# Performance work log

Hardware: AMD Instinct MI355X
Metric: run time of the kernel (lower is better)

The kernel has to match this reference:

```python
import jax, jax.numpy as jnp
import numpy as np

H = 256      # hidden_dim
F_IN = 32    # infeat_dim1 + infeat_dim2 (shared 'feat')
P = 8192     # nodes per topo level
L = 16       # topo levels; level 0 = PIs, last level = POs
FANIN = 8    # uniform in-degree (dense mailbox)


def _mlp(x, w1, b1, w2, b2):
    # MLP(sizes...) = Linear -> LeakyReLU(0.1) -> Linear
    return jax.nn.leaky_relu(x @ w1 + b1, 0.1) @ w2 + b2


def setup_inputs() -> dict:
    key = jax.random.key(0)
    ks = jax.random.split(key, 24)
    w = lambda k, s: jax.random.normal(k, s, jnp.float32) * 0.1
    z = lambda n: jnp.zeros((n,), jnp.float32)
    return {
        "delay": jax.random.uniform(ks[0], (P, 1), jnp.float32),
        "feat": jax.random.normal(ks[1], (L * P, F_IN), jnp.float32),
        "bit_pos": jax.random.uniform(ks[2], (L - 1, P, FANIN), jnp.float32),
        "po_feat": jax.random.uniform(ks[3], (P, 1), jnp.float32),
        "src_idx": jax.random.randint(ks[4], (L - 1, P, FANIN), 0, P, jnp.int32),
        # mlp_pi: 1 -> H/2 -> H
        "pi_w1": w(ks[5], (1, H // 2)), "pi_b1": z(H // 2),
        "pi_w2": w(ks[6], (H // 2, H)), "pi_b2": z(H),
        # mlp_neigh_gate: (H + F_IN) -> H/2 -> H
        "gate_w1": w(ks[7], (H + F_IN, H // 2)), "gate_b1": z(H // 2),
        "gate_w2": w(ks[8], (H // 2, H)), "gate_b2": z(H),
        # mlp_neigh_module: (H + F_IN + 1) -> H/2 -> H
        "mod_w1": w(ks[9], (H + F_IN + 1, H // 2)), "mod_b1": z(H // 2),
        "mod_w2": w(ks[10], (H // 2, H)), "mod_b2": z(H),
        # mlp_type: F_IN -> 32 -> 32
        "type_w1": w(ks[11], (F_IN, 32)), "type_b1": z(32),
        "type_w2": w(ks[12], (32, 32)), "type_b2": z(32),
        # mlp_pos: 1 -> 32 -> 32
        "pos_w1": w(ks[13], (1, 32)), "pos_b1": z(32),
        "pos_w2": w(ks[14], (32, 32)), "pos_b2": z(32),
        "attn_vec_m": w(ks[15], (H + 64, 1)),
        # mlp_global: 1 -> H/2 -> H
        "glob_w1": w(ks[16], (1, H // 2)), "glob_b1": z(H // 2),
        "glob_w2": w(ks[17], (H // 2, H)), "glob_b2": z(H),
        # mlp_out: 2H -> H -> 1
        "out_w1": w(ks[18], (2 * H, H)), "out_b1": z(H),
        "out_w2": w(ks[19], (H, 1)), "out_b2": z(1),
    }


def reference(delay, feat, bit_pos, po_feat,
              pi_w1, pi_b1, pi_w2, pi_b2,
              gate_w1, gate_b1, gate_w2, gate_b2,
              mod_w1, mod_b1, mod_w2, mod_b2,
              type_w1, type_b1, type_w2, type_b2,
              pos_w1, pos_b1, pos_w2, pos_b2,
              attn_vec_m,
              glob_w1, glob_b1, glob_w2, glob_b2,
              out_w1, out_b1, out_w2, out_b2,
              src_idx):
    L1, P_, F_ = src_idx.shape  # levels beyond PIs
    Pg = P_ // 2                # first half gates, second half modules
    # level 0: nodes_func_pi -> h = mlp_pi(delay)
    prev_h = _mlp(delay, pi_w1, pi_b1, pi_w2, pi_b2)  # [P, H]
    for l in range(L1):
        sh = prev_h[src_idx[l]]                    # gather src h: [P, F, H]
        lvl_feat = feat[(l + 1) * P_:(l + 2) * P_]  # [P, F_IN]
        # --- gates: reduce_func_smoothmax + nodes_func_gate ---
        mg = sh[:Pg]                               # mailbox [Pg, F, H]
        neigh_g = jnp.sum(mg * jax.nn.softmax(mg, axis=1), axis=1)  # [Pg, H]
        hg = _mlp(jnp.concatenate([neigh_g, lvl_feat[:Pg]], axis=1),
                  gate_w1, gate_b1, gate_w2, gate_b2)
        # --- modules: edge_msg_module + reduce_func_attn + nodes_func_module ---
        sm = sh[Pg:]                               # [Pm, F, H]
        dstf = lvl_feat[Pg:]                       # [Pm, F_IN]
        zt = _mlp(dstf, type_w1, type_b1, type_w2, type_b2)          # [Pm, 32]
        bp = bit_pos[l, Pg:]                       # [Pm, F]
        zp = _mlp(bp[..., None], pos_w1, pos_b1, pos_w2, pos_b2)     # [Pm, F, 32]
        z = jnp.concatenate(
            [jnp.broadcast_to(zt[:, None, :], zp.shape), zp, sm], axis=-1)  # [Pm, F, H+64]
        alpha = jax.nn.softmax(z @ attn_vec_m, axis=1)               # [Pm, F, 1]
        m = jnp.concatenate([sm, bp[..., None]], axis=-1)            # [Pm, F, H+1]
        neigh_m = jnp.sum(alpha * m, axis=1)                         # [Pm, H+1]
        hm = _mlp(jnp.concatenate([neigh_m, dstf], axis=1),
                  mod_w1, mod_b1, mod_w2, mod_b2)
        hl = jnp.concatenate([hg, hm], axis=0)     # [P, H]
        # ReLU where is_po != 1; only last level nodes are POs
        prev_h = hl if l == L1 - 1 else jax.nn.relu(hl)
    # POs = entire last level; flag_global concat
    h_global = _mlp(po_feat, glob_w1, glob_b1, glob_w2, glob_b2)  # [P, H]
    h = jnp.concatenate([prev_h, h_global], axis=1)               # [P, 2H]
    return _mlp(h, out_w1, out_b1, out_w2, out_b2)                # [P, 1]
```

## Files before the change

kernel.cpp:

```cpp
#include <hip/hip_runtime.h>
#include <math.h>

#define HD   256
#define FIN  32
#define NP   8192
#define PGH  4096
#define NLVL 15
#define TN   16

typedef __attribute__((ext_vector_type(4))) short v4s;
typedef __attribute__((ext_vector_type(8))) short v8s;
typedef __attribute__((ext_vector_type(4))) float v4f;

#define MFMA __builtin_amdgcn_mfma_f32_16x16x32_bf16

__device__ __align__(16) unsigned short g_wpk[606208];

__device__ __forceinline__ float lrelu(float x) { return x > 0.f ? x : 0.1f * x; }

__device__ __forceinline__ void cvt_duo(float v, unsigned short& hi, unsigned short& lo) {
    unsigned int u = __float_as_uint(v);
    unsigned int r = u + 0x7fffu + ((u >> 16) & 1u);
    hi = (unsigned short)(r >> 16);
    float d = v - __uint_as_float((unsigned int)hi << 16);
    unsigned int u2 = __float_as_uint(d);
    unsigned int r2 = u2 + 0x7fffu + ((u2 >> 16) & 1u);
    lo = (unsigned short)(r2 >> 16);
}

__device__ __forceinline__ v8s pack8(v4s a, v4s b) {
    v8s r; r[0]=a[0]; r[1]=a[1]; r[2]=a[2]; r[3]=a[3]; r[4]=b[0]; r[5]=b[1]; r[6]=b[2]; r[7]=b[3];
    return r;
}

__global__ __launch_bounds__(256) void prep_kernel(
    const float* __restrict__ gw1, const float* __restrict__ mw1,
    const float* __restrict__ gw2, const float* __restrict__ mw2,
    const float* __restrict__ glw2, const float* __restrict__ ow1)
{
    int t = blockIdx.x * 256 + threadIdx.x;
    const float* src; int base, N, idx;
    if (t < 36864)       { src = gw1;  base = 0;      N = 128; idx = t; }
    else if (t < 73728)  { src = mw1;  base = 73728;  N = 128; idx = t - 36864; }
    else if (t < 106496) { src = gw2;  base = 147456; N = 256; idx = t - 73728; }
    else if (t < 139264) { src = mw2;  base = 212992; N = 256; idx = t - 106496; }
    else if (t < 172032) { src = glw2; base = 278528; N = 256; idx = t - 139264; }
    else if (t < 303104) { src = ow1;  base = 344064; N = 256; idx = t - 172032; }
    else return;
    int sh = (N == 128) ? 7 : 8;
    int k = idx >> sh, col = idx & (N - 1);
    float v = src[idx];
    unsigned short hi, lo; cvt_duo(v, hi, lo);
    int ks = k >> 5, kk = k & 31;
    int ch = col >> 7, cc = col & 127, ct = cc >> 4;
    int nch = N >> 7;
    int l = ((kk & 15) >> 2) * 16 + (cc & 15);
    int w = (kk & 3) + (kk >> 4) * 4;
    int off = ((ks * nch + ch) * 2) * 4096 + ct * 512 + l * 8 + w;
    g_wpk[base + off] = hi;
    g_wpk[base + off + 4096] = lo;
}

__global__ __launch_bounds__(256) void pi_kernel(
    const float* __restrict__ delay,
    const float* __restrict__ w1, const float* __restrict__ b1,
    const float* __restrict__ w2, const float* __restrict__ b2,
    const float* __restrict__ av,
    float* __restrict__ outh, float* __restrict__ sdot)
{
    __shared__ float g1[TN][132];
    const int tid = threadIdx.x;
    const int node0 = blockIdx.x * TN;

    for (int t = tid; t < TN * 128; t += 256) {
        int i = t >> 7, jj = t & 127;
        g1[i][jj] = lrelu(delay[node0 + i] * w1[jj] + b1[jj]);
    }
    __syncthreads();

    const int j = (tid & 63) * 4;
    const int rg = (tid >> 6) * 4;
    float acc[4][4];
    float4 bv = *(const float4*)&b2[j];
#pragma unroll
    for (int ri = 0; ri < 4; ri++) { acc[ri][0] = bv.x; acc[ri][1] = bv.y; acc[ri][2] = bv.z; acc[ri][3] = bv.w; }

#pragma unroll 2
    for (int k = 0; k < 128; k += 4) {
        float4 x0 = *(const float4*)&g1[rg + 0][k];
        float4 x1 = *(const float4*)&g1[rg + 1][k];
        float4 x2v = *(const float4*)&g1[rg + 2][k];
        float4 x3 = *(const float4*)&g1[rg + 3][k];
        const float* wp = w2 + (size_t)k * 256 + j;
#define PIK(comp, off) { float4 wv = *(const float4*)(wp + (off) * 256); \
    acc[0][0] += x0.comp * wv.x; acc[0][1] += x0.comp * wv.y; acc[0][2] += x0.comp * wv.z; acc[0][3] += x0.comp * wv.w; \
    acc[1][0] += x1.comp * wv.x; acc[1][1] += x1.comp * wv.y; acc[1][2] += x1.comp * wv.z; acc[1][3] += x1.comp * wv.w; \
    acc[2][0] += x2v.comp * wv.x; acc[2][1] += x2v.comp * wv.y; acc[2][2] += x2v.comp * wv.z; acc[2][3] += x2v.comp * wv.w; \
    acc[3][0] += x3.comp * wv.x; acc[3][1] += x3.comp * wv.y; acc[3][2] += x3.comp * wv.z; acc[3][3] += x3.comp * wv.w; }
        PIK(x, 0) PIK(y, 1) PIK(z, 2) PIK(w, 3)
#undef PIK
    }
    float4 avj = *(const float4*)&av[64 + j];
#pragma unroll
    for (int ri = 0; ri < 4; ri++) {
        *(float4*)&outh[(node0 + rg + ri) * HD + j] =
            make_float4(acc[ri][0], acc[ri][1], acc[ri][2], acc[ri][3]);
        float p = acc[ri][0] * avj.x + acc[ri][1] * avj.y + acc[ri][2] * avj.z + acc[ri][3] * avj.w;
#pragma unroll
        for (int off = 1; off < 64; off <<= 1) p += __shfl_xor(p, off);
        if ((tid & 63) == 0) sdot[node0 + rg + ri] = p;
    }
}

__global__ __launch_bounds__(512, 4) void level_kernel(
    const float* __restrict__ prevh, float* __restrict__ nexth,
    const float* __restrict__ sdot_prev, float* __restrict__ sdot_next,
    const float* __restrict__ feat, const float* __restrict__ bitpos,
    const int* __restrict__ srcidx,
    const float* __restrict__ g_w1, const float* __restrict__ g_b1,
    const float* __restrict__ g_b2,
    const float* __restrict__ m_w1, const float* __restrict__ m_b1,
    const float* __restrict__ m_b2,
    const float* __restrict__ t_w1, const float* __restrict__ t_b1,
    const float* __restrict__ t_w2, const float* __restrict__ t_b2,
    const float* __restrict__ p_w1, const float* __restrict__ p_b1,
    const float* __restrict__ p_w2, const float* __restrict__ p_b2,
    const float* __restrict__ av,
    int level, int apply_relu)
{
    __shared__ unsigned short xh_lds[16 * 296];
    __shared__ unsigned short xl_lds[16 * 296];
    __shared__ unsigned short h1h_lds[16 * 136];
    __shared__ unsigned short h1l_lds[16 * 136];
    __shared__ float wbuf[2][4096];
    __shared__ int   src_lds[128];
    __shared__ float bp_lds[128];
    __shared__ float dstf_lds[16][32];
    __shared__ float ztt_lds[16][32];
    __shared__ float alpha_lds[128];
    __shared__ float xbp_lds[16];
    __shared__ float av_lds[64];
    __shared__ float tw2av_lds[32];
    __shared__ float pw2av_lds[32];
    __shared__ float bias_av[2];
    __shared__ float red_lds[16][8];

    const int tid = threadIdx.x;
    const bool is_gate = (blockIdx.x < 256);
    const int node0 = is_gate ? (blockIdx.x * TN) : (PGH + ((int)blockIdx.x - 256) * TN);

    const float* w1 = is_gate ? g_w1 : m_w1;
    const float* b1 = is_gate ? g_b1 : m_b1;
    const float* b2 = is_gate ? g_b2 : m_b2;
    const float4* gpk1 = (const float4*)(g_wpk + (is_gate ? 0 : 73728));
    const float4* gpk2 = (const float4*)(g_wpk + (is_gate ? 147456 : 212992));

    float4 ta = gpk1[tid], tb = gpk1[512 + tid];

    if (tid < 128) src_lds[tid] = srcidx[(level * NP + node0) * 8 + tid];

    if (is_gate) {
        {
            int i = tid >> 5, k = tid & 31;
            float v = feat[((level + 1) * NP + node0 + i) * FIN + k];
            unsigned short h, l; cvt_duo(v, h, l);
            xh_lds[i * 296 + 256 + k] = h; xl_lds[i * 296 + 256 + k] = l;
        }
        __syncthreads();
        {
            const int c = tid & 255, sh = (tid >> 8) * 8;
            for (int s0 = 0; s0 < 8; s0 += 4) {
                const int* spA = &src_lds[(sh + s0 + 0) * 8];
                const int* spB = &src_lds[(sh + s0 + 1) * 8];
                const int* spC = &src_lds[(sh + s0 + 2) * 8];
                const int* spD = &src_lds[(sh + s0 + 3) * 8];
                float ma[8], mb[8], mc[8], md[8];
#pragma unroll
                for (int f = 0; f < 8; f++) ma[f] = prevh[spA[f] * HD + c];
#pragma unroll
                for (int f = 0; f < 8; f++) mb[f] = prevh[spB[f] * HD + c];
#pragma unroll
                for (int f = 0; f < 8; f++) mc[f] = prevh[spC[f] * HD + c];
#pragma unroll
                for (int f = 0; f < 8; f++) md[f] = prevh[spD[f] * HD + c];
                float mxa = -1e30f, mxb = -1e30f, mxc = -1e30f, mxd = -1e30f;
#pragma unroll
                for (int f = 0; f < 8; f++) {
                    mxa = fmaxf(mxa, ma[f]); mxb = fmaxf(mxb, mb[f]);
                    mxc = fmaxf(mxc, mc[f]); mxd = fmaxf(mxd, md[f]);
                }
                float sa = 0.f, wsa = 0.f, sb = 0.f, wsb = 0.f;
                float sc = 0.f, wsc = 0.f, sd = 0.f, wsd = 0.f;
#pragma unroll
                for (int f = 0; f < 8; f++) {
                    float ea = __expf(ma[f] - mxa); sa += ea; wsa += ma[f] * ea;
                    float eb = __expf(mb[f] - mxb); sb += eb; wsb += mb[f] * eb;
                    float ec = __expf(mc[f] - mxc); sc += ec; wsc += mc[f] * ec;
                    float ed = __expf(md[f] - mxd); sd += ed; wsd += md[f] * ed;
                }
                unsigned short h, l;
                cvt_duo(wsa / sa, h, l); xh_lds[(sh+s0+0)*296 + c] = h; xl_lds[(sh+s0+0)*296 + c] = l;
                cvt_duo(wsb / sb, h, l); xh_lds[(sh+s0+1)*296 + c] = h; xl_lds[(sh+s0+1)*296 + c] = l;
                cvt_duo(wsc / sc, h, l); xh_lds[(sh+s0+2)*296 + c] = h; xl_lds[(sh+s0+2)*296 + c] = l;
                cvt_duo(wsd / sd, h, l); xh_lds[(sh+s0+3)*296 + c] = h; xl_lds[(sh+s0+3)*296 + c] = l;
            }
        }
        __syncthreads();
    } else {
        if (tid < 128) bp_lds[tid] = bitpos[(level * NP + node0) * 8 + tid];
        {
            int i = tid >> 5, k = tid & 31;
            float v = feat[((level + 1) * NP + node0 + i) * FIN + k];
            dstf_lds[i][k] = v;
            unsigned short h, l; cvt_duo(v, h, l);
            xh_lds[i * 296 + 257 + k] = h; xl_lds[i * 296 + 257 + k] = l;
        }
        if (tid < 64) av_lds[tid] = av[tid];
        __syncthreads();

        {
            int i = tid >> 5, jj = tid & 31;
            float a = t_b1[jj];
#pragma unroll 8
            for (int k = 0; k < 32; k++) a += dstf_lds[i][k] * t_w1[k * 32 + jj];
            ztt_lds[i][jj] = lrelu(a);
        }
        if (tid < 32) {
            float s = 0.f;
#pragma unroll 8
            for (int jj = 0; jj < 32; jj++) s += t_w2[tid * 32 + jj] * av_lds[jj];
            tw2av_lds[tid] = s;
        } else if (tid < 64) {
            int k = tid - 32;
            float s = 0.f;
#pragma unroll 8
            for (int jj = 0; jj < 32; jj++) s += p_w2[k * 32 + jj] * av_lds[32 + jj];
            pw2av_lds[k] = s;
        } else if (tid == 64) {
            float s = 0.f;
#pragma unroll 8
            for (int jj = 0; jj < 32; jj++) s += t_b2[jj] * av_lds[jj];
            bias_av[0] = s;
        } else if (tid == 65) {
            float s = 0.f;
#pragma unroll 8
            for (int jj = 0; jj < 32; jj++) s += p_b2[jj] * av_lds[32 + jj];
            bias_av[1] = s;
        }
        __syncthreads();

        if (tid < 256) {
            const int jg = tid & 1, f = (tid >> 1) & 7, i = tid >> 4;
            const float sv = sdot_prev[src_lds[i * 8 + f]];
            const float bpv = bp_lds[i * 8 + f];
            float part = 0.f;
            const int k0 = jg * 16;
#pragma unroll
            for (int k = k0; k < k0 + 16; k++) {
                float h1pk = lrelu(bpv * p_w1[k] + p_b1[k]);
                part += h1pk * pw2av_lds[k];
                part += ztt_lds[i][k] * tw2av_lds[k];
            }
            part += __shfl_xor(part, 1);
            float logit = part + bias_av[0] + bias_av[1] + sv;
            float mx = logit;
            mx = fmaxf(mx, __shfl_xor(mx, 2));
            mx = fmaxf(mx, __shfl_xor(mx, 4));
            mx = fmaxf(mx, __shfl_xor(mx, 8));
            float e = __expf(logit - mx);
            float ssum = e;
            ssum += __shfl_xor(ssum, 2);
            ssum += __shfl_xor(ssum, 4);
            ssum += __shfl_xor(ssum, 8);
            float alpha = e / ssum;
            if (jg == 0) alpha_lds[i * 8 + f] = alpha;
            float ab = alpha * bpv;
            ab += __shfl_xor(ab, 2);
            ab += __shfl_xor(ab, 4);
            ab += __shfl_xor(ab, 8);
            if ((tid & 15) == 0) xbp_lds[i] = ab;
        }
        __syncthreads();

        {
            const int c = tid & 255, sh = (tid >> 8) * 8;
            for (int s0 = 0; s0 < 8; s0 += 4) {
                const int* spA = &src_lds[(sh + s0 + 0) * 8];
                const int* spB = &src_lds[(sh + s0 + 1) * 8];
                const int* spC = &src_lds[(sh + s0 + 2) * 8];
                const int* spD = &src_lds[(sh + s0 + 3) * 8];
                float ma[8], mb[8], mc[8], md[8];
#pragma unroll
                for (int f = 0; f < 8; f++) ma[f] = prevh[spA[f] * HD + c];
#pragma unroll
                for (int f = 0; f < 8; f++) mb[f] = prevh[spB[f] * HD + c];
#pragma unroll
                for (int f = 0; f < 8; f++) mc[f] = prevh[spC[f] * HD + c];
#pragma unroll
                for (int f = 0; f < 8; f++) md[f] = prevh[spD[f] * HD + c];
                const float* apA = &alpha_lds[(sh + s0 + 0) * 8];
                const float* apB = &alpha_lds[(sh + s0 + 1) * 8];
                const float* apC = &alpha_lds[(sh + s0 + 2) * 8];
                const float* apD = &alpha_lds[(sh + s0 + 3) * 8];
                float aa = 0.f, ab2 = 0.f, ac = 0.f, ad = 0.f;
#pragma unroll
                for (int f = 0; f < 8; f++) {
                    aa  += apA[f] * ma[f]; ab2 += apB[f] * mb[f];
                    ac  += apC[f] * mc[f]; ad  += apD[f] * md[f];
                }
                unsigned short h, l;
                cvt_duo(aa,  h, l); xh_lds[(sh+s0+0)*296 + c] = h; xl_lds[(sh+s0+0)*296 + c] = l;
                cvt_duo(ab2, h, l); xh_lds[(sh+s0+1)*296 + c] = h; xl_lds[(sh+s0+1)*296 + c] = l;
                cvt_duo(ac,  h, l); xh_lds[(sh+s0+2)*296 + c] = h; xl_lds[(sh+s0+2)*296 + c] = l;
                cvt_duo(ad,  h, l); xh_lds[(sh+s0+3)*296 + c] = h; xl_lds[(sh+s0+3)*296 + c] = l;
            }
        }
        if (tid < TN) {
            unsigned short h, l; cvt_duo(xbp_lds[tid], h, l);
            xh_lds[tid * 296 + 256] = h; xl_lds[tid * 296 + 256] = l;
        }
        __syncthreads();
    }

    const int lane = tid & 63, wv = tid >> 6;
    const int lr = lane & 15, lg = lane >> 4;

    {
        const unsigned short* xrh = xh_lds + lr * 296 + 4 * lg;
        const unsigned short* xrl = xl_lds + lr * 296 + 4 * lg;
        const int colg = wv * 16 + lr;
        float bb = b1[colg];
        v4f acc = {bb, bb, bb, bb};
        for (int s = 0; s < 9; ++s) {
            float4* w4 = (float4*)wbuf[s & 1];
            w4[tid] = ta; w4[tid + 512] = tb;
            if (s < 8) { ta = gpk1[(s + 1) * 1024 + tid]; tb = gpk1[(s + 1) * 1024 + 512 + tid]; }
            __syncthreads();
            const unsigned short* wb = (const unsigned short*)wbuf[s & 1];
            int k0 = s * 32;
            v8s Ah = pack8(*(const v4s*)(xrh + k0), *(const v4s*)(xrh + k0 + 16));
            v8s Al = pack8(*(const v4s*)(xrl + k0), *(const v4s*)(xrl + k0 + 16));
            v8s Bh = *(const v8s*)(wb + wv * 512 + lane * 8);
            v8s Bl = *(const v8s*)(wb + 4096 + wv * 512 + lane * 8);
            acc = MFMA(Ah, Bh, acc, 0, 0, 0);
            acc = MFMA(Ah, Bl, acc, 0, 0, 0);
            acc = MFMA(Al, Bh, acc, 0, 0, 0);
        }
        ta = gpk2[tid]; tb = gpk2[512 + tid];
        float w288 = is_gate ? 0.f : w1[288 * 128 + colg];
#pragma unroll
        for (int r = 0; r < 4; ++r) {
            int row = lg * 4 + r;
            float v = acc[r];
            if (!is_gate) v += dstf_lds[row][31] * w288;
            v = lrelu(v);
            unsigned short h, l; cvt_duo(v, h, l);
            h1h_lds[row * 136 + colg] = h;
            h1l_lds[row * 136 + colg] = l;
        }
    }
    __syncthreads();

    {
        const unsigned short* h1rh = h1h_lds + lr * 136 + 4 * lg;
        const unsigned short* h1rl = h1l_lds + lr * 136 + 4 * lg;
        const int col0 = wv * 16 + lr;
        float bb0 = b2[col0], bb1 = b2[128 + col0];
        v4f acc0 = {bb0, bb0, bb0, bb0};
        v4f acc1 = {bb1, bb1, bb1, bb1};
        v8s Ah = {0,0,0,0,0,0,0,0}, Al = {0,0,0,0,0,0,0,0};
#pragma unroll
        for (int s = 0; s < 8; ++s) {
            float4* w4 = (float4*)wbuf[s & 1];
            w4[tid] = ta; w4[tid + 512] = tb;
            if (s < 7) { ta = gpk2[(s + 1) * 1024 + tid]; tb = gpk2[(s + 1) * 1024 + 512 + tid]; }
            __syncthreads();
            const unsigned short* wb = (const unsigned short*)wbuf[s & 1];
            if ((s & 1) == 0) {
                int k0 = (s >> 1) * 32;
                Ah = pack8(*(const v4s*)(h1rh + k0), *(const v4s*)(h1rh + k0 + 16));
                Al = pack8(*(const v4s*)(h1rl + k0), *(const v4s*)(h1rl + k0 + 16));
            }
            v8s Bh = *(const v8s*)(wb + wv * 512 + lane * 8);
            v8s Bl = *(const v8s*)(wb + 4096 + wv * 512 + lane * 8);
            if ((s & 1) == 0) {
                acc0 = MFMA(Ah, Bh, acc0, 0, 0, 0);
                acc0 = MFMA(Ah, Bl, acc0, 0, 0, 0);
                acc0 = MFMA(Al, Bh, acc0, 0, 0, 0);
            } else {
                acc1 = MFMA(Ah, Bh, acc1, 0, 0, 0);
                acc1 = MFMA(Ah, Bl, acc1, 0, 0, 0);
                acc1 = MFMA(Al, Bh, acc1, 0, 0, 0);
            }
        }
        float pr[4] = {0.f, 0.f, 0.f, 0.f};
#pragma unroll
        for (int r = 0; r < 4; ++r) {
            int row = lg * 4 + r;
            float v = acc0[r];
            if (apply_relu) v = fmaxf(v, 0.f);
            nexth[(node0 + row) * HD + col0] = v;
            pr[r] += v * av[64 + col0];
            float v2 = acc1[r];
            if (apply_relu) v2 = fmaxf(v2, 0.f);
            nexth[(node0 + row) * HD + 128 + col0] = v2;
            pr[r] += v2 * av[192 + col0];
        }
#pragma unroll
        for (int off = 1; off < 16; off <<= 1) {
#pragma unroll
            for (int r = 0; r < 4; ++r) pr[r] += __shfl_xor(pr[r], off);
        }
        if (lr == 0) {
#pragma unroll
            for (int r = 0; r < 4; ++r) red_lds[lg * 4 + r][wv] = pr[r];
        }
        __syncthreads();
        if (tid < TN) {
            float s = 0.f;
#pragma unroll
            for (int w = 0; w < 8; w++) s += red_lds[tid][w];
            sdot_next[node0 + tid] = s;
        }
    }
}

__global__ __launch_bounds__(512, 4) void final_kernel(
    const float* __restrict__ prevh, const float* __restrict__ pofeat,
    const float* __restrict__ gl_w1, const float* __restrict__ gl_b1,
    const float* __restrict__ gl_b2,
    const float* __restrict__ o_b1,
    const float* __restrict__ o_w2, const float* __restrict__ o_b2,
    float* __restrict__ out)
{
    __shared__ unsigned short x2h[16 * 520];
    __shared__ unsigned short x2l[16 * 520];
    __shared__ unsigned short g1h[16 * 136];
    __shared__ unsigned short g1l[16 * 136];
    __shared__ float wbuf[2][4096];
    __shared__ float ow2_lds[256];
    __shared__ float red_lds[16][8];

    const int tid = threadIdx.x;
    const int node0 = blockIdx.x * TN;
    const float4* gpkG = (const float4*)(g_wpk + 278528);
    const float4* gpkO = (const float4*)(g_wpk + 344064);
    float4 ta = gpkG[tid], tb = gpkG[512 + tid];

    for (int q = tid; q < TN * 64; q += 512) {
        int i = q >> 6, c4 = (q & 63) * 4;
        float4 v = *(const float4*)&prevh[(node0 + i) * HD + c4];
        unsigned short h, l;
        cvt_duo(v.x, h, l); x2h[i * 520 + c4 + 0] = h; x2l[i * 520 + c4 + 0] = l;
        cvt_duo(v.y, h, l); x2h[i * 520 + c4 + 1] = h; x2l[i * 520 + c4 + 1] = l;
        cvt_duo(v.z, h, l); x2h[i * 520 + c4 + 2] = h; x2l[i * 520 + c4 + 2] = l;
        cvt_duo(v.w, h, l); x2h[i * 520 + c4 + 3] = h; x2l[i * 520 + c4 + 3] = l;
    }
    for (int t = tid; t < TN * 128; t += 512) {
        int i = t >> 7, jj = t & 127;
        float v = lrelu(pofeat[node0 + i] * gl_w1[jj] + gl_b1[jj]);
        unsigned short h, l; cvt_duo(v, h, l);
        g1h[i * 136 + jj] = h; g1l[i * 136 + jj] = l;
    }
    if (tid < 256) ow2_lds[tid] = o_w2[tid];
    __syncthreads();

    const int lane = tid & 63, wv = tid >> 6;
    const int lr = lane & 15, lg = lane >> 4;
    const int col0 = wv * 16 + lr;

    {
        const unsigned short* grh = g1h + lr * 136 + 4 * lg;
        const unsigned short* grl = g1l + lr * 136 + 4 * lg;
        float bb0 = gl_b2[col0], bb1 = gl_b2[128 + col0];
        v4f acc0 = {bb0, bb0, bb0, bb0};
        v4f acc1 = {bb1, bb1, bb1, bb1};
        v8s Ah = {0,0,0,0,0,0,0,0}, Al = {0,0,0,0,0,0,0,0};
#pragma unroll
        for (int s = 0; s < 8; ++s) {
            float4* w4 = (float4*)wbuf[s & 1];
            w4[tid] = ta; w4[tid + 512] = tb;
            if (s < 7) { ta = gpkG[(s + 1) * 1024 + tid]; tb = gpkG[(s + 1) * 1024 + 512 + tid]; }
            else       { ta = gpkO[tid]; tb = gpkO[512 + tid]; }
            __syncthreads();
            const unsigned short* wb = (const unsigned short*)wbuf[s & 1];
            if ((s & 1) == 0) {
                int k0 = (s >> 1) * 32;
                Ah = pack8(*(const v4s*)(grh + k0), *(const v4s*)(grh + k0 + 16));
                Al = pack8(*(const v4s*)(grl + k0), *(const v4s*)(grl + k0 + 16));
            }
            v8s Bh = *(const v8s*)(wb + wv * 512 + lane * 8);
            v8s Bl = *(const v8s*)(wb + 4096 + wv * 512 + lane * 8);
            if ((s & 1) == 0) {
                acc0 = MFMA(Ah, Bh, acc0, 0, 0, 0);
                acc0 = MFMA(Ah, Bl, acc0, 0, 0, 0);
                acc0 = MFMA(Al, Bh, acc0, 0, 0, 0);
            } else {
                acc1 = MFMA(Ah, Bh, acc1, 0, 0, 0);
                acc1 = MFMA(Ah, Bl, acc1, 0, 0, 0);
                acc1 = MFMA(Al, Bh, acc1, 0, 0, 0);
            }
        }
#pragma unroll
        for (int r = 0; r < 4; ++r) {
            int row = lg * 4 + r;
            unsigned short h, l;
            cvt_duo(acc0[r], h, l); x2h[row * 520 + 256 + col0] = h; x2l[row * 520 + 256 + col0] = l;
            cvt_duo(acc1[r], h, l); x2h[row * 520 + 384 + col0] = h; x2l[row * 520 + 384 + col0] = l;
        }
    }
    __syncthreads();

    {
        const unsigned short* xrh = x2h + lr * 520 + 4 * lg;
        const unsigned short* xrl = x2l + lr * 520 + 4 * lg;
        float bb0 = o_b1[col0], bb1 = o_b1[128 + col0];
        v4f acc0 = {bb0, bb0, bb0, bb0};
        v4f acc1 = {bb1, bb1, bb1, bb1};
        v8s Ah = {0,0,0,0,0,0,0,0}, Al = {0,0,0,0,0,0,0,0};
        for (int s = 0; s < 32; ++s) {
            float4* w4 = (float4*)wbuf[s & 1];
            w4[tid] = ta; w4[tid + 512] = tb;
            if (s < 31) { ta = gpkO[(s + 1) * 1024 + tid]; tb = gpkO[(s + 1) * 1024 + 512 + tid]; }
            __syncthreads();
            const unsigned short* wb = (const unsigned short*)wbuf[s & 1];
            if ((s & 1) == 0) {
                int k0 = (s >> 1) * 32;
                Ah = pack8(*(const v4s*)(xrh + k0), *(const v4s*)(xrh + k0 + 16));
                Al = pack8(*(const v4s*)(xrl + k0), *(const v4s*)(xrl + k0 + 16));
            }
            v8s Bh = *(const v8s*)(wb + wv * 512 + lane * 8);
            v8s Bl = *(const v8s*)(wb + 4096 + wv * 512 + lane * 8);
            if ((s & 1) == 0) {
                acc0 = MFMA(Ah, Bh, acc0, 0, 0, 0);
                acc0 = MFMA(Ah, Bl, acc0, 0, 0, 0);
                acc0 = MFMA(Al, Bh, acc0, 0, 0, 0);
            } else {
                acc1 = MFMA(Ah, Bh, acc1, 0, 0, 0);
                acc1 = MFMA(Ah, Bl, acc1, 0, 0, 0);
                acc1 = MFMA(Al, Bh, acc1, 0, 0, 0);
            }
        }
        float pr[4] = {0.f, 0.f, 0.f, 0.f};
#pragma unroll
        for (int r = 0; r < 4; ++r) {
            pr[r] += lrelu(acc0[r]) * ow2_lds[col0];
            pr[r] += lrelu(acc1[r]) * ow2_lds[128 + col0];
        }
#pragma unroll
        for (int off = 1; off < 16; off <<= 1) {
#pragma unroll
            for (int r = 0; r < 4; ++r) pr[r] += __shfl_xor(pr[r], off);
        }
        if (lr == 0) {
#pragma unroll
            for (int r = 0; r < 4; ++r) red_lds[lg * 4 + r][wv] = pr[r];
        }
        __syncthreads();
        if (tid < TN) {
            float s = 0.f;
#pragma unroll
            for (int w = 0; w < 8; w++) s += red_lds[tid][w];
            out[node0 + tid] = s + o_b2[0];
        }
    }
}

extern "C" void kernel_launch(void* const* d_in, const int* in_sizes, int n_in,
                              void* d_out, int out_size, void* d_ws, size_t ws_size,
                              hipStream_t stream)
{
    const float* delay    = (const float*)d_in[0];
    const float* feat     = (const float*)d_in[1];
    const float* bitpos   = (const float*)d_in[2];
    const float* pofeat   = (const float*)d_in[3];
    const int*   srcidx   = (const int*)  d_in[4];
    const float* pi_w1    = (const float*)d_in[5];
    const float* pi_b1    = (const float*)d_in[6];
    const float* pi_w2    = (const float*)d_in[7];
    const float* pi_b2    = (const float*)d_in[8];
    const float* gate_w1  = (const float*)d_in[9];
    const float* gate_b1  = (const float*)d_in[10];
    const float* gate_w2  = (const float*)d_in[11];
    const float* gate_b2  = (const float*)d_in[12];
    const float* mod_w1   = (const float*)d_in[13];
    const float* mod_b1   = (const float*)d_in[14];
    const float* mod_w2   = (const float*)d_in[15];
    const float* mod_b2   = (const float*)d_in[16];
    const float* type_w1  = (const float*)d_in[17];
    const float* type_b1  = (const float*)d_in[18];
    const float* type_w2  = (const float*)d_in[19];
    const float* type_b2  = (const float*)d_in[20];
    const float* pos_w1   = (const float*)d_in[21];
    const float* pos_b1   = (const float*)d_in[22];
    const float* pos_w2   = (const float*)d_in[23];
    const float* pos_b2   = (const float*)d_in[24];
    const float* attn_vec = (const float*)d_in[25];
    const float* glob_w1  = (const float*)d_in[26];
    const float* glob_b1  = (const float*)d_in[27];
    const float* glob_w2  = (const float*)d_in[28];
    const float* glob_b2  = (const float*)d_in[29];
    const float* out_w1   = (const float*)d_in[30];
    const float* out_b1   = (const float*)d_in[31];
    const float* out_w2   = (const float*)d_in[32];
    const float* out_b2   = (const float*)d_in[33];

    float* buf0 = (float*)d_ws;
    float* buf1 = buf0 + (size_t)NP * HD;
    float* sd0  = buf1 + (size_t)NP * HD;
    float* sd1  = sd0 + NP;

    prep_kernel<<<1184, 256, 0, stream>>>(gate_w1, mod_w1, gate_w2, mod_w2, glob_w2, out_w1);

    pi_kernel<<<NP / TN, 256, 0, stream>>>(delay, pi_w1, pi_b1, pi_w2, pi_b2,
                                           attn_vec, buf0, sd0);

    for (int l = 0; l < NLVL; l++) {
        float* pv = (l & 1) ? buf1 : buf0;
        float* nx = (l & 1) ? buf0 : buf1;
        float* sp = (l & 1) ? sd1 : sd0;
        float* sn = (l & 1) ? sd0 : sd1;
        level_kernel<<<NP / TN, 512, 0, stream>>>(
            pv, nx, sp, sn, feat, bitpos, srcidx,
            gate_w1, gate_b1, gate_b2,
            mod_w1, mod_b1, mod_b2,
            type_w1, type_b1, type_w2, type_b2,
            pos_w1, pos_b1, pos_w2, pos_b2,
            attn_vec, l, (l != NLVL - 1) ? 1 : 0);
    }

    final_kernel<<<NP / TN, 512, 0, stream>>>(
        buf1, pofeat,
        glob_w1, glob_b1, glob_b2,
        out_b1, out_w2, out_b2,
        (float*)d_out);
}
```

Baseline: 347.2 us.

## Load packed MFMA weight fragments directly from global instead of LDS staging

Removes the double-buffered LDS weight staging (wbuf) and its per-step __syncthreads in both the level kernel and the output kernel. Each wave now reads its B fragments straight from the pre-packed global weight array, which should be served from L2 or L1. This drops block-wide barriers and 32 KB of LDS per block, which may allow more resident blocks. The cost is more global/L2 traffic, since each wave fetches its own slice with no sharing through LDS, and load latency is no longer hidden by an explicit prefetch.

```diff
diff --git a/kernel.cpp b/kernel.cpp
--- a/kernel.cpp
+++ b/kernel.cpp
@@ -132,7 +132,6 @@
     __shared__ unsigned short xl_lds[16 * 296];
     __shared__ unsigned short h1h_lds[16 * 136];
     __shared__ unsigned short h1l_lds[16 * 136];
-    __shared__ float wbuf[2][4096];
     __shared__ int   src_lds[128];
     __shared__ float bp_lds[128];
     __shared__ float dstf_lds[16][32];
@@ -152,10 +151,8 @@
     const float* w1 = is_gate ? g_w1 : m_w1;
     const float* b1 = is_gate ? g_b1 : m_b1;
     const float* b2 = is_gate ? g_b2 : m_b2;
-    const float4* gpk1 = (const float4*)(g_wpk + (is_gate ? 0 : 73728));
-    const float4* gpk2 = (const float4*)(g_wpk + (is_gate ? 147456 : 212992));
-
-    float4 ta = gpk1[tid], tb = gpk1[512 + tid];
+    const unsigned short* pk1 = g_wpk + (is_gate ? 0 : 73728);
+    const unsigned short* pk2 = g_wpk + (is_gate ? 147456 : 212992);
 
     if (tid < 128) src_lds[tid] = srcidx[(level * NP + node0) * 8 + tid];
 
@@ -331,22 +328,18 @@
         const int colg = wv * 16 + lr;
         float bb = b1[colg];
         v4f acc = {bb, bb, bb, bb};
+#pragma unroll
         for (int s = 0; s < 9; ++s) {
-            float4* w4 = (float4*)wbuf[s & 1];
-            w4[tid] = ta; w4[tid + 512] = tb;
-            if (s < 8) { ta = gpk1[(s + 1) * 1024 + tid]; tb = gpk1[(s + 1) * 1024 + 512 + tid]; }
-            __syncthreads();
-            const unsigned short* wb = (const unsigned short*)wbuf[s & 1];
+            const unsigned short* wb = pk1 + s * 8192 + wv * 512 + lane * 8;
+            v8s Bh = *(const v8s*)(wb);
+            v8s Bl = *(const v8s*)(wb + 4096);
             int k0 = s * 32;
             v8s Ah = pack8(*(const v4s*)(xrh + k0), *(const v4s*)(xrh + k0 + 16));
             v8s Al = pack8(*(const v4s*)(xrl + k0), *(const v4s*)(xrl + k0 + 16));
-            v8s Bh = *(const v8s*)(wb + wv * 512 + lane * 8);
-            v8s Bl = *(const v8s*)(wb + 4096 + wv * 512 + lane * 8);
             acc = MFMA(Ah, Bh, acc, 0, 0, 0);
             acc = MFMA(Ah, Bl, acc, 0, 0, 0);
             acc = MFMA(Al, Bh, acc, 0, 0, 0);
         }
-        ta = gpk2[tid]; tb = gpk2[512 + tid];
         float w288 = is_gate ? 0.f : w1[288 * 128 + colg];
 #pragma unroll
         for (int r = 0; r < 4; ++r) {
@@ -368,30 +361,23 @@
         float bb0 = b2[col0], bb1 = b2[128 + col0];
         v4f acc0 = {bb0, bb0, bb0, bb0};
         v4f acc1 = {bb1, bb1, bb1, bb1};
-        v8s Ah = {0,0,0,0,0,0,0,0}, Al = {0,0,0,0,0,0,0,0};
-#pragma unroll
-        for (int s = 0; s < 8; ++s) {
-            float4* w4 = (float4*)wbuf[s & 1];
-            w4[tid] = ta; w4[tid + 512] = tb;
-            if (s < 7) { ta = gpk2[(s + 1) * 1024 + tid]; tb = gpk2[(s + 1) * 1024 + 512 + tid]; }
-            __syncthreads();
-            const unsigned short* wb = (const unsigned short*)wbuf[s & 1];
-            if ((s & 1) == 0) {
-                int k0 = (s >> 1) * 32;
-                Ah = pack8(*(const v4s*)(h1rh + k0), *(const v4s*)(h1rh + k0 + 16));
-                Al = pack8(*(const v4s*)(h1rl + k0), *(const v4s*)(h1rl + k0 + 16));
-            }
-            v8s Bh = *(const v8s*)(wb + wv * 512 + lane * 8);
-            v8s Bl = *(const v8s*)(wb + 4096 + wv * 512 + lane * 8);
-            if ((s & 1) == 0) {
-                acc0 = MFMA(Ah, Bh, acc0, 0, 0, 0);
-                acc0 = MFMA(Ah, Bl, acc0, 0, 0, 0);
-                acc0 = MFMA(Al, Bh, acc0, 0, 0, 0);
-            } else {
-                acc1 = MFMA(Ah, Bh, acc1, 0, 0, 0);
-                acc1 = MFMA(Ah, Bl, acc1, 0, 0, 0);
-                acc1 = MFMA(Al, Bh, acc1, 0, 0, 0);
-            }
+#pragma unroll
+        for (int ks = 0; ks < 4; ++ks) {
+            int k0 = ks * 32;
+            v8s Ah = pack8(*(const v4s*)(h1rh + k0), *(const v4s*)(h1rh + k0 + 16));
+            v8s Al = pack8(*(const v4s*)(h1rl + k0), *(const v4s*)(h1rl + k0 + 16));
+            const unsigned short* wb0 = pk2 + (ks * 2 + 0) * 8192 + wv * 512 + lane * 8;
+            const unsigned short* wb1 = pk2 + (ks * 2 + 1) * 8192 + wv * 512 + lane * 8;
+            v8s Bh0 = *(const v8s*)(wb0);
+            v8s Bl0 = *(const v8s*)(wb0 + 4096);
+            v8s Bh1 = *(const v8s*)(wb1);
+            v8s Bl1 = *(const v8s*)(wb1 + 4096);
+            acc0 = MFMA(Ah, Bh0, acc0, 0, 0, 0);
+            acc0 = MFMA(Ah, Bl0, acc0, 0, 0, 0);
+            acc0 = MFMA(Al, Bh0, acc0, 0, 0, 0);
+            acc1 = MFMA(Ah, Bh1, acc1, 0, 0, 0);
+            acc1 = MFMA(Ah, Bl1, acc1, 0, 0, 0);
+            acc1 = MFMA(Al, Bh1, acc1, 0, 0, 0);
         }
         float pr[4] = {0.f, 0.f, 0.f, 0.f};
 #pragma unroll
@@ -437,15 +423,13 @@
     __shared__ unsigned short x2l[16 * 520];
     __shared__ unsigned short g1h[16 * 136];
     __shared__ unsigned short g1l[16 * 136];
-    __shared__ float wbuf[2][4096];
     __shared__ float ow2_lds[256];
     __shared__ float red_lds[16][8];
 
     const int tid = threadIdx.x;
     const int node0 = blockIdx.x * TN;
-    const float4* gpkG = (const float4*)(g_wpk + 278528);
-    const float4* gpkO = (const float4*)(g_wpk + 344064);
-    float4 ta = gpkG[tid], tb = gpkG[512 + tid];
+    const unsigned short* pkG = g_wpk + 278528;
+    const unsigned short* pkO = g_wpk + 344064;
 
     for (int q = tid; q < TN * 64; q += 512) {
         int i = q >> 6, c4 = (q & 63) * 4;
@@ -475,31 +459,23 @@
         float bb0 = gl_b2[col0], bb1 = gl_b2[128 + col0];
         v4f acc0 = {bb0, bb0, bb0, bb0};
         v4f acc1 = {bb1, bb1, bb1, bb1};
-        v8s Ah = {0,0,0,0,0,0,0,0}, Al = {0,0,0,0,0,0,0,0};
-#pragma unroll
-        for (int s = 0; s < 8; ++s) {
-            float4* w4 = (float4*)wbuf[s & 1];
-            w4[tid] = ta; w4[tid + 512] = tb;
-            if (s < 7) { ta = gpkG[(s + 1) * 1024 + tid]; tb = gpkG[(s + 1) * 1024 + 512 + tid]; }
-            else       { ta = gpkO[tid]; tb = gpkO[512 + tid]; }
-            __syncthreads();
-            const unsigned short* wb = (const unsigned short*)wbuf[s & 1];
-            if ((s & 1) == 0) {
-                int k0 = (s >> 1) * 32;
-                Ah = pack8(*(const v4s*)(grh + k0), *(const v4s*)(grh + k0 + 16));
-                Al = pack8(*(const v4s*)(grl + k0), *(const v4s*)(grl + k0 + 16));
-            }
-            v8s Bh = *(const v8s*)(wb + wv * 512 + lane * 8);
-            v8s Bl = *(const v8s*)(wb + 4096 + wv * 512 + lane * 8);
-            if ((s & 1) == 0) {
-                acc0 = MFMA(Ah, Bh, acc0, 0, 0, 0);
-                acc0 = MFMA(Ah, Bl, acc0, 0, 0, 0);
-                acc0 = MFMA(Al, Bh, acc0, 0, 0, 0);
-            } else {
-                acc1 = MFMA(Ah, Bh, acc1, 0, 0, 0);
-                acc1 = MFMA(Ah, Bl, acc1, 0, 0, 0);
-                acc1 = MFMA(Al, Bh, acc1, 0, 0, 0);
-            }
+#pragma unroll
+        for (int ks = 0; ks < 4; ++ks) {
+            int k0 = ks * 32;
+            v8s Ah = pack8(*(const v4s*)(grh + k0), *(const v4s*)(grh + k0 + 16));
+            v8s Al = pack8(*(const v4s*)(grl + k0), *(const v4s*)(grl + k0 + 16));
+            const unsigned short* wb0 = pkG + (ks * 2 + 0) * 8192 + wv * 512 + lane * 8;
+            const unsigned short* wb1 = pkG + (ks * 2 + 1) * 8192 + wv * 512 + lane * 8;
+            v8s Bh0 = *(const v8s*)(wb0);
+            v8s Bl0 = *(const v8s*)(wb0 + 4096);
+            v8s Bh1 = *(const v8s*)(wb1);
+            v8s Bl1 = *(const v8s*)(wb1 + 4096);
+            acc0 = MFMA(Ah, Bh0, acc0, 0, 0, 0);
+            acc0 = MFMA(Ah, Bl0, acc0, 0, 0, 0);
+            acc0 = MFMA(Al, Bh0, acc0, 0, 0, 0);
+            acc1 = MFMA(Ah, Bh1, acc1, 0, 0, 0);
+            acc1 = MFMA(Ah, Bl1, acc1, 0, 0, 0);
+            acc1 = MFMA(Al, Bh1, acc1, 0, 0, 0);
         }
 #pragma unroll
         for (int r = 0; r < 4; ++r) {
@@ -517,29 +493,22 @@
         float bb0 = o_b1[col0], bb1 = o_b1[128 + col0];
         v4f acc0 = {bb0, bb0, bb0, bb0};
         v4f acc1 = {bb1, bb1, bb1, bb1};
-        v8s Ah = {0,0,0,0,0,0,0,0}, Al = {0,0,0,0,0,0,0,0};
-        for (int s = 0; s < 32; ++s) {
-            float4* w4 = (float4*)wbuf[s & 1];
-            w4[tid] = ta; w4[tid + 512] = tb;
-            if (s < 31) { ta = gpkO[(s + 1) * 1024 + tid]; tb = gpkO[(s + 1) * 1024 + 512 + tid]; }
-            __syncthreads();
-            const unsigned short* wb = (const unsigned short*)wbuf[s & 1];
-            if ((s & 1) == 0) {
-                int k0 = (s >> 1) * 32;
-                Ah = pack8(*(const v4s*)(xrh + k0), *(const v4s*)(xrh + k0 + 16));
-                Al = pack8(*(const v4s*)(xrl + k0), *(const v4s*)(xrl + k0 + 16));
-            }
-            v8s Bh = *(const v8s*)(wb + wv * 512 + lane * 8);
-            v8s Bl = *(const v8s*)(wb + 4096 + wv * 512 + lane * 8);
-            if ((s & 1) == 0) {
-                acc0 = MFMA(Ah, Bh, acc0, 0, 0, 0);
-                acc0 = MFMA(Ah, Bl, acc0, 0, 0, 0);
-                acc0 = MFMA(Al, Bh, acc0, 0, 0, 0);
-            } else {
-                acc1 = MFMA(Ah, Bh, acc1, 0, 0, 0);
-                acc1 = MFMA(Ah, Bl, acc1, 0, 0, 0);
-                acc1 = MFMA(Al, Bh, acc1, 0, 0, 0);
-            }
+        for (int ks = 0; ks < 16; ++ks) {
+            int k0 = ks * 32;
+            v8s Ah = pack8(*(const v4s*)(xrh + k0), *(const v4s*)(xrh + k0 + 16));
+            v8s Al = pack8(*(const v4s*)(xrl + k0), *(const v4s*)(xrl + k0 + 16));
+            const unsigned short* wb0 = pkO + (ks * 2 + 0) * 8192 + wv * 512 + lane * 8;
+            const unsigned short* wb1 = pkO + (ks * 2 + 1) * 8192 + wv * 512 + lane * 8;
+            v8s Bh0 = *(const v8s*)(wb0);
+            v8s Bl0 = *(const v8s*)(wb0 + 4096);
+            v8s Bh1 = *(const v8s*)(wb1);
+            v8s Bl1 = *(const v8s*)(wb1 + 4096);
+            acc0 = MFMA(Ah, Bh0, acc0, 0, 0, 0);
+            acc0 = MFMA(Ah, Bl0, acc0, 0, 0, 0);
+            acc0 = MFMA(Al, Bh0, acc0, 0, 0, 0);
+            acc1 = MFMA(Ah, Bh1, acc1, 0, 0, 0);
+            acc1 = MFMA(Ah, Bl1, acc1, 0, 0, 0);
+            acc1 = MFMA(Al, Bh1, acc1, 0, 0, 0);
         }
         float pr[4] = {0.f, 0.f, 0.f, 0.f};
 #pragma unroll
```

New measurement: 313.6 us. 9.7% less time.
